# Performance work log

Hardware: AMD Instinct MI355X
Metric: run time of the kernel (lower is better)

## Reference

```python
import jax, jax.numpy as jnp
import numpy as np

B, D, T, BINS = 8, 768, 16384, 1024

def setup_inputs() -> dict:
    key = jax.random.key(0)
    k1, k2, k3, k4 = jax.random.split(key, 4)
    ssl_content = jax.random.normal(k1, (B, D, T), dtype=jnp.float32)
    conv_w = jax.random.normal(k2, (D, D, 2), dtype=jnp.float32) * 0.02  # Conv1d(768,768,k=2,s=2) weight [out,in,k]
    conv_b = jax.random.normal(k3, (D,), dtype=jnp.float32) * 0.02
    codebook = jax.random.normal(k4, (BINS, D), dtype=jnp.float32)
    return {"ssl_content": ssl_content, "conv_w": conv_w, "conv_b": conv_b, "codebook": codebook}

def reference(ssl_content, conv_w, conv_b, codebook):
    # ssl_proj: Conv1d(D, D, kernel_size=2, stride=2), no padding
    ssl = jax.lax.conv_general_dilated(
        ssl_content, conv_w, window_strides=(2,), padding='VALID',
        dimension_numbers=('NCH', 'OIH', 'NCH')) + conv_b[None, :, None]  # [B, D, T//2]
    x = jnp.transpose(ssl, (0, 2, 1))            # b d n -> b n d : [B, T', D]
    b, tq, d = x.shape
    flat = x.reshape(-1, d)                      # [B*T', D]
    # Euclidean codebook search: argmin_k ||flat - codebook[k]||^2
    d2 = (jnp.sum(flat * flat, axis=-1, keepdims=True)
          - 2.0 * (flat @ codebook.T)
          + jnp.sum(codebook * codebook, axis=-1))  # [B*T', BINS]
    codes = jnp.argmin(d2, axis=-1).reshape(b, tq)  # n_q=1 -> indices for quantizer 0: [B, T']
    prompt = codes[0][None, :]                   # codes[0,0].unsqueeze(0) -> [1, T']
    return prompt
```

## Files before the change

kernel.cpp:

```cpp
#include <hip/hip_runtime.h>

#define D    768
#define T    16384
#define TQ   8192
#define BINS 1024
#define K1   1536
#define NKA  (K1 / 32)
#define NKS  (D / 32)
#define FRAG 1024

typedef _Float16 f16;
typedef _Float16 h8 __attribute__((ext_vector_type(8)));
typedef float    f32x4 __attribute__((ext_vector_type(4)));


__device__ __forceinline__ void gl_lds16(const void* g, void* l) {
    __builtin_amdgcn_global_load_lds(
        (const __attribute__((address_space(1))) void*)g,
        (__attribute__((address_space(3))) void*)l, 16, 0, 0);
}

__global__ __launch_bounds__(64) void cnorm_kernel(const float* __restrict__ cb,
                                                   float* __restrict__ cnorm) {
    int bin  = blockIdx.x;
    int lane = threadIdx.x;
    const float* row = cb + bin * D;
    float s = 0.f;
    for (int k = lane; k < D; k += 64) { float v = row[k]; s += v * v; }
    #pragma unroll
    for (int off = 32; off > 0; off >>= 1) s += __shfl_down(s, off);
    if (lane == 0) cnorm[bin] = s;
}

__global__ __launch_bounds__(256) void pack_b_kernel(
    const float* __restrict__ src, f16* __restrict__ hi, f16* __restrict__ lo,
    int K, int nfrag) {
    int wid = threadIdx.x >> 6, lane = threadIdx.x & 63;
    int fid = blockIdx.x * 4 + wid;
    if (fid >= nfrag) return;
    int nk = K >> 5;
    int r16 = fid / nk, kblk = fid - r16 * nk;
    int row = r16 * 16 + (lane & 15);
    int k0  = kblk * 32 + 8 * (lane >> 4);
    const float* s = src + (size_t)row * K + k0;
    float4 v0 = *(const float4*)s;
    float4 v1 = *(const float4*)(s + 4);
    float vv[8] = {v0.x, v0.y, v0.z, v0.w, v1.x, v1.y, v1.z, v1.w};
    h8 vh, vl;
    #pragma unroll
    for (int j = 0; j < 8; ++j) {
        f16 h = (f16)vv[j];
        vh[j] = h;
        vl[j] = (f16)((vv[j] - (float)h) * 2048.f);
    }
    size_t off = ((size_t)fid * 64 + lane) * 8;
    *(h8*)&hi[off] = vh;
    *(h8*)&lo[off] = vl;
}

__global__ __launch_bounds__(256) void pack_a_kernel(const float* __restrict__ ssl,
                                                     f16* __restrict__ hi,
                                                     f16* __restrict__ lo) {
    int wid = threadIdx.x >> 6, lane = threadIdx.x & 63;
    int kblk = blockIdx.x;
    int l15 = lane & 15, lk = lane >> 4;
    #pragma unroll
    for (int q = 0; q < 2; ++q) {
        int tblk = blockIdx.y * 8 + wid * 2 + q;
        int tp = tblk * 16 + l15;
        int i0 = kblk * 16 + 4 * lk;
        float vv[8];
        #pragma unroll
        for (int ii = 0; ii < 4; ++ii) {
            float2 v = *(const float2*)&ssl[(size_t)(i0 + ii) * T + 2 * tp];
            vv[2 * ii]     = v.x;
            vv[2 * ii + 1] = v.y;
        }
        h8 vh, vl;
        #pragma unroll
        for (int j = 0; j < 8; ++j) {
            f16 h = (f16)vv[j];
            vh[j] = h;
            vl[j] = (f16)((vv[j] - (float)h) * 2048.f);
        }
        size_t off = ((size_t)(tblk * NKA + kblk) * 64 + lane) * 8;
        *(h8*)&hi[off] = vh;
        *(h8*)&lo[off] = vl;
    }
}

__global__ __launch_bounds__(256, 2) void conv_mfma_kernel(
    const f16* __restrict__ Ah, const f16* __restrict__ Al,
    const f16* __restrict__ Bh, const f16* __restrict__ Bl,
    const float* __restrict__ bias,
    f16* __restrict__ Xhi, f16* __restrict__ Xlo)
{
    __shared__ __align__(16) char smem[32768];
    int tid = threadIdx.x, lane = tid & 63, wid = tid >> 6;
    int wm = wid >> 1, wn = wid & 1;
    int l15 = lane & 15, lk = lane >> 4;
    int mb = blockIdx.y * 128, nb = blockIdx.x * 128;
    int mb16 = mb >> 4, nb16 = nb >> 4;

    const f16* gsrc; int blk16;
    if      (wid == 0) { gsrc = Ah; blk16 = mb16; }
    else if (wid == 1) { gsrc = Al; blk16 = mb16; }
    else if (wid == 2) { gsrc = Bh; blk16 = nb16; }
    else               { gsrc = Bl; blk16 = nb16; }
    const char* gw = (const char*)gsrc + (size_t)blk16 * NKA * FRAG + lane * 16;
    char* lw = smem + wid * 8192;

    const f32x4 zero4 = {0.f, 0.f, 0.f, 0.f};
    f32x4 acc[4][4];
    #pragma unroll
    for (int i = 0; i < 4; ++i)
        #pragma unroll
        for (int j = 0; j < 4; ++j) acc[i][j] = zero4;

    for (int kblk = 0; kblk < NKA; ++kblk) {
        __syncthreads();
        #pragma unroll
        for (int f = 0; f < 8; ++f)
            gl_lds16(gw + (size_t)(f * NKA + kblk) * FRAG, lw + f * FRAG);
        __syncthreads();
        h8 ah[4], al[4];
        #pragma unroll
        for (int mf = 0; mf < 4; ++mf) {
            int fo = (wm * 4 + mf) * FRAG + lane * 16;
            ah[mf] = *(const h8*)(smem + fo);
            al[mf] = *(const h8*)(smem + 8192 + fo);
        }
        #pragma unroll
        for (int nf = 0; nf < 4; ++nf) {
            int fo = (wn * 4 + nf) * FRAG + lane * 16;
            h8 bh = *(const h8*)(smem + 16384 + fo);
            h8 bl = *(const h8*)(smem + 24576 + fo);
            #pragma unroll
            for (int mf = 0; mf < 4; ++mf) {
                acc[mf][nf] = __builtin_amdgcn_mfma_f32_16x16x32_f16(ah[mf], bh, acc[mf][nf], 0, 0, 0);
                f32x4 t = __builtin_amdgcn_mfma_f32_16x16x32_f16(ah[mf], bl, zero4, 0, 0, 0);
                t = __builtin_amdgcn_mfma_f32_16x16x32_f16(al[mf], bh, t, 0, 0, 0);
                acc[mf][nf] += t * 4.8828125e-4f;
            }
        }
    }

    float* sb = (float*)smem;
    float bv[4];
    #pragma unroll
    for (int nf = 0; nf < 4; ++nf) bv[nf] = bias[nb + wn * 64 + nf * 16 + l15];
    #pragma unroll
    for (int s = 0; s < 4; ++s) {
        __syncthreads();
        if (wm == (s >> 1)) {
            #pragma unroll
            for (int mh = 0; mh < 2; ++mh) {
                int mf = (s & 1) * 2 + mh;
                int srow = mh * 16 + lk * 4;
                #pragma unroll
                for (int nf = 0; nf < 4; ++nf) {
                    int scol = wn * 64 + nf * 16 + l15;
                    #pragma unroll
                    for (int r = 0; r < 4; ++r)
                        sb[(srow + r) * 132 + scol] = acc[mf][nf][r] + bv[nf];
                }
            }
        }
        __syncthreads();
        #pragma unroll
        for (int h = 0; h < 2; ++h) {
            int f = wid * 2 + h;
            int tl = f & 1, dbl = f >> 1;
            int srow = tl * 16 + l15;
            int sd   = dbl * 32 + 8 * lk;
            float vv[8];
            #pragma unroll
            for (int j = 0; j < 8; ++j) vv[j] = sb[srow * 132 + sd + j];
            h8 vh, vl;
            #pragma unroll
            for (int j = 0; j < 8; ++j) {
                f16 hh = (f16)vv[j];
                vh[j] = hh;
                vl[j] = (f16)((vv[j] - (float)hh) * 2048.f);
            }
            int tblk_g = mb16 + s * 2 + tl;
            int dblk_g = (nb >> 5) + dbl;
            size_t off = ((size_t)(tblk_g * NKS + dblk_g) * 64 + lane) * 8;
            *(h8*)&Xhi[off] = vh;
            *(h8*)&Xlo[off] = vl;
        }
    }
}

__global__ __launch_bounds__(256, 2) void score_mfma_kernel(
    const f16* __restrict__ Ah, const f16* __restrict__ Al,
    const f16* __restrict__ Bh, const f16* __restrict__ Bl,
    const float* __restrict__ cnorm,
    float* __restrict__ pval, int* __restrict__ pidx)
{
    __shared__ __align__(16) char smem[32768];
    int tid = threadIdx.x, lane = tid & 63, wid = tid >> 6;
    int wm = wid >> 1, wn = wid & 1;
    int l15 = lane & 15, lk = lane >> 4;
    int mb = blockIdx.y * 128, nb = blockIdx.x * 128;
    int mb16 = mb >> 4, nb16 = nb >> 4;

    const f16* gsrc; int blk16;
    if      (wid == 0) { gsrc = Ah; blk16 = mb16; }
    else if (wid == 1) { gsrc = Al; blk16 = mb16; }
    else if (wid == 2) { gsrc = Bh; blk16 = nb16; }
    else               { gsrc = Bl; blk16 = nb16; }
    const char* gw = (const char*)gsrc + (size_t)blk16 * NKS * FRAG + lane * 16;
    char* lw = smem + wid * 8192;

    const f32x4 zero4 = {0.f, 0.f, 0.f, 0.f};
    f32x4 acc[4][4];
    #pragma unroll
    for (int i = 0; i < 4; ++i)
        #pragma unroll
        for (int j = 0; j < 4; ++j) acc[i][j] = zero4;

    for (int kblk = 0; kblk < NKS; ++kblk) {
        __syncthreads();
        #pragma unroll
        for (int f = 0; f < 8; ++f)
            gl_lds16(gw + (size_t)(f * NKS + kblk) * FRAG, lw + f * FRAG);
        __syncthreads();
        h8 ah[4], al[4];
        #pragma unroll
        for (int mf = 0; mf < 4; ++mf) {
            int fo = (wm * 4 + mf) * FRAG + lane * 16;
            ah[mf] = *(const h8*)(smem + fo);
            al[mf] = *(const h8*)(smem + 8192 + fo);
        }
        #pragma unroll
        for (int nf = 0; nf < 4; ++nf) {
            int fo = (wn * 4 + nf) * FRAG + lane * 16;
            h8 bh = *(const h8*)(smem + 16384 + fo);
            h8 bl = *(const h8*)(smem + 24576 + fo);
            #pragma unroll
            for (int mf = 0; mf < 4; ++mf) {
                acc[mf][nf] = __builtin_amdgcn_mfma_f32_16x16x32_f16(ah[mf], bh, acc[mf][nf], 0, 0, 0);
                f32x4 t = __builtin_amdgcn_mfma_f32_16x16x32_f16(ah[mf], bl, zero4, 0, 0, 0);
                t = __builtin_amdgcn_mfma_f32_16x16x32_f16(al[mf], bh, t, 0, 0, 0);
                acc[mf][nf] += t * 4.8828125e-4f;
            }
        }
    }
    float cn[4];
    #pragma unroll
    for (int nf = 0; nf < 4; ++nf) cn[nf] = cnorm[nb + wn * 64 + nf * 16 + l15];
    int slice = blockIdx.x * 2 + wn;
    #pragma unroll
    for (int mf = 0; mf < 4; ++mf) {
        #pragma unroll
        for (int r = 0; r < 4; ++r) {
            float v = 3.4e38f; int ix = 0;
            #pragma unroll
            for (int nf = 0; nf < 4; ++nf) {
                float sc = cn[nf] - 2.f * acc[mf][nf][r];
                int col = nb + wn * 64 + nf * 16 + l15;
                if (sc < v) { v = sc; ix = col; }
            }
            #pragma unroll
            for (int off = 8; off > 0; off >>= 1) {
                float ov = __shfl_xor(v, off);
                int   oi = __shfl_xor(ix, off);
                if (ov < v || (ov == v && oi < ix)) { v = ov; ix = oi; }
            }
            if (l15 == 0) {
                int row = mb + wm * 64 + mf * 16 + lk * 4 + r;
                pval[row * 16 + slice] = v;
                pidx[row * 16 + slice] = ix;
            }
        }
    }
}

__global__ __launch_bounds__(256) void argmin_final_kernel(
    const float* __restrict__ pval, const int* __restrict__ pidx,
    int* __restrict__ out)
{
    int r = blockIdx.x * 256 + threadIdx.x;
    float best = 3.4e38f; int bi = 0;
    #pragma unroll
    for (int s = 0; s < 16; ++s) {
        float v = pval[r * 16 + s];
        if (v < best) { best = v; bi = pidx[r * 16 + s]; }
    }
    out[r] = bi;
}

extern "C" void kernel_launch(void* const* d_in, const int* in_sizes, int n_in,
                              void* d_out, int out_size, void* d_ws, size_t ws_size,
                              hipStream_t stream) {
    const float* ssl = (const float*)d_in[0];
    const float* W   = (const float*)d_in[1];
    const float* bia = (const float*)d_in[2];
    const float* cb  = (const float*)d_in[3];
    int* out = (int*)d_out;

    char* p = (char*)d_ws;
    float* cnorm = (float*)p;  p += 4096;
    f16* Whi  = (f16*)p;  p += (size_t)D * K1 * 2;
    f16* Wlo  = (f16*)p;  p += (size_t)D * K1 * 2;
    f16* CBhi = (f16*)p;  p += (size_t)BINS * D * 2;
    f16* CBlo = (f16*)p;  p += (size_t)BINS * D * 2;
    f16* Ahi  = (f16*)p;  p += (size_t)TQ * K1 * 2;
    f16* Alo  = (f16*)p;  p += (size_t)TQ * K1 * 2;
    f16* Xhi  = (f16*)p;  p += (size_t)TQ * D * 2;
    f16* Xlo  = (f16*)p;  p += (size_t)TQ * D * 2;
    float* pval = (float*)p;  p += (size_t)TQ * 16 * 4;
    int*   pidx = (int*)p;    p += (size_t)TQ * 16 * 4;

    cnorm_kernel<<<BINS, 64, 0, stream>>>(cb, cnorm);
    pack_b_kernel<<<(48 * 48) / 4, 256, 0, stream>>>(W, Whi, Wlo, K1, 48 * 48);
    pack_b_kernel<<<(64 * 24) / 4, 256, 0, stream>>>(cb, CBhi, CBlo, D, 64 * 24);
    pack_a_kernel<<<dim3(NKA, TQ / 128), 256, 0, stream>>>(ssl, Ahi, Alo);
    conv_mfma_kernel<<<dim3(D / 128, TQ / 128), 256, 0, stream>>>(
        Ahi, Alo, Whi, Wlo, bia, Xhi, Xlo);
    score_mfma_kernel<<<dim3(BINS / 128, TQ / 128), 256, 0, stream>>>(
        Xhi, Xlo, CBhi, CBlo, cnorm, pval, pidx);
    argmin_final_kernel<<<TQ / 256, 256, 0, stream>>>(pval, pidx, out);
}
```

Baseline: 587.7 us.

## Double-buffer LDS tiles and accumulate correction terms in separate MFMA accumulators

Both GEMM kernels (conv and score) now use two LDS buffers, so the global-to-LDS load for the next k-block is issued before computing on the current one. This replaces two barriers per iteration with one. The hi/lo correction products are also accumulated in a second accumulator array and scaled once in the epilogue, instead of zero-init MFMAs plus a vector multiply-add every step. This doubles accumulator registers and LDS per block (64KB), which may reduce occupancy below the launch-bounds target of 2 blocks per CU.

Result: faster. 562.0 us (-4.4%).

```diff
diff --git a/kernel.cpp b/kernel.cpp
--- a/kernel.cpp
+++ b/kernel.cpp
@@ -95,7 +95,7 @@
     const float* __restrict__ bias,
     f16* __restrict__ Xhi, f16* __restrict__ Xlo)
 {
-    __shared__ __align__(16) char smem[32768];
+    __shared__ __align__(16) char smem[65536];
     int tid = threadIdx.x, lane = tid & 63, wid = tid >> 6;
     int wm = wid >> 1, wn = wid & 1;
     int l15 = lane & 15, lk = lane >> 4;
@@ -108,41 +108,51 @@
     else if (wid == 2) { gsrc = Bh; blk16 = nb16; }
     else               { gsrc = Bl; blk16 = nb16; }
     const char* gw = (const char*)gsrc + (size_t)blk16 * NKA * FRAG + lane * 16;
-    char* lw = smem + wid * 8192;
+    char* lw0 = smem + wid * 8192;
+    char* lw1 = smem + 32768 + wid * 8192;
 
     const f32x4 zero4 = {0.f, 0.f, 0.f, 0.f};
-    f32x4 acc[4][4];
+    f32x4 acc[4][4], acc2[4][4];
     #pragma unroll
     for (int i = 0; i < 4; ++i)
         #pragma unroll
-        for (int j = 0; j < 4; ++j) acc[i][j] = zero4;
-
+        for (int j = 0; j < 4; ++j) { acc[i][j] = zero4; acc2[i][j] = zero4; }
+
+    #pragma unroll
+    for (int f = 0; f < 8; ++f)
+        gl_lds16(gw + (size_t)(f * NKA) * FRAG, lw0 + f * FRAG);
+    __syncthreads();
+
+    int cur = 0;
     for (int kblk = 0; kblk < NKA; ++kblk) {
-        __syncthreads();
-        #pragma unroll
-        for (int f = 0; f < 8; ++f)
-            gl_lds16(gw + (size_t)(f * NKA + kblk) * FRAG, lw + f * FRAG);
-        __syncthreads();
+        if (kblk + 1 < NKA) {
+            char* lwn = cur ? lw0 : lw1;
+            #pragma unroll
+            for (int f = 0; f < 8; ++f)
+                gl_lds16(gw + (size_t)(f * NKA + kblk + 1) * FRAG, lwn + f * FRAG);
+        }
+        const char* base = smem + cur * 32768;
         h8 ah[4], al[4];
         #pragma unroll
         for (int mf = 0; mf < 4; ++mf) {
             int fo = (wm * 4 + mf) * FRAG + lane * 16;
-            ah[mf] = *(const h8*)(smem + fo);
-            al[mf] = *(const h8*)(smem + 8192 + fo);
+            ah[mf] = *(const h8*)(base + fo);
+            al[mf] = *(const h8*)(base + 8192 + fo);
         }
         #pragma unroll
         for (int nf = 0; nf < 4; ++nf) {
             int fo = (wn * 4 + nf) * FRAG + lane * 16;
-            h8 bh = *(const h8*)(smem + 16384 + fo);
-            h8 bl = *(const h8*)(smem + 24576 + fo);
+            h8 bh = *(const h8*)(base + 16384 + fo);
+            h8 bl = *(const h8*)(base + 24576 + fo);
             #pragma unroll
             for (int mf = 0; mf < 4; ++mf) {
-                acc[mf][nf] = __builtin_amdgcn_mfma_f32_16x16x32_f16(ah[mf], bh, acc[mf][nf], 0, 0, 0);
-                f32x4 t = __builtin_amdgcn_mfma_f32_16x16x32_f16(ah[mf], bl, zero4, 0, 0, 0);
-                t = __builtin_amdgcn_mfma_f32_16x16x32_f16(al[mf], bh, t, 0, 0, 0);
-                acc[mf][nf] += t * 4.8828125e-4f;
-            }
-        }
+                acc [mf][nf] = __builtin_amdgcn_mfma_f32_16x16x32_f16(ah[mf], bh, acc [mf][nf], 0, 0, 0);
+                acc2[mf][nf] = __builtin_amdgcn_mfma_f32_16x16x32_f16(ah[mf], bl, acc2[mf][nf], 0, 0, 0);
+                acc2[mf][nf] = __builtin_amdgcn_mfma_f32_16x16x32_f16(al[mf], bh, acc2[mf][nf], 0, 0, 0);
+            }
+        }
+        __syncthreads();
+        cur ^= 1;
     }
 
     float* sb = (float*)smem;
@@ -162,7 +172,8 @@
                     int scol = wn * 64 + nf * 16 + l15;
                     #pragma unroll
                     for (int r = 0; r < 4; ++r)
-                        sb[(srow + r) * 132 + scol] = acc[mf][nf][r] + bv[nf];
+                        sb[(srow + r) * 132 + scol] =
+                            acc[mf][nf][r] + acc2[mf][nf][r] * 4.8828125e-4f + bv[nf];
                 }
             }
         }
@@ -198,7 +209,7 @@
     const float* __restrict__ cnorm,
     float* __restrict__ pval, int* __restrict__ pidx)
 {
-    __shared__ __align__(16) char smem[32768];
+    __shared__ __align__(16) char smem[65536];
     int tid = threadIdx.x, lane = tid & 63, wid = tid >> 6;
     int wm = wid >> 1, wn = wid & 1;
     int l15 = lane & 15, lk = lane >> 4;
@@ -211,41 +222,51 @@
     else if (wid == 2) { gsrc = Bh; blk16 = nb16; }
     else               { gsrc = Bl; blk16 = nb16; }
     const char* gw = (const char*)gsrc + (size_t)blk16 * NKS * FRAG + lane * 16;
-    char* lw = smem + wid * 8192;
+    char* lw0 = smem + wid * 8192;
+    char* lw1 = smem + 32768 + wid * 8192;
 
     const f32x4 zero4 = {0.f, 0.f, 0.f, 0.f};
-    f32x4 acc[4][4];
+    f32x4 acc[4][4], acc2[4][4];
     #pragma unroll
     for (int i = 0; i < 4; ++i)
         #pragma unroll
-        for (int j = 0; j < 4; ++j) acc[i][j] = zero4;
-
+        for (int j = 0; j < 4; ++j) { acc[i][j] = zero4; acc2[i][j] = zero4; }
+
+    #pragma unroll
+    for (int f = 0; f < 8; ++f)
+        gl_lds16(gw + (size_t)(f * NKS) * FRAG, lw0 + f * FRAG);
+    __syncthreads();
+
+    int cur = 0;
     for (int kblk = 0; kblk < NKS; ++kblk) {
-        __syncthreads();
-        #pragma unroll
-        for (int f = 0; f < 8; ++f)
-            gl_lds16(gw + (size_t)(f * NKS + kblk) * FRAG, lw + f * FRAG);
-        __syncthreads();
+        if (kblk + 1 < NKS) {
+            char* lwn = cur ? lw0 : lw1;
+            #pragma unroll
+            for (int f = 0; f < 8; ++f)
+                gl_lds16(gw + (size_t)(f * NKS + kblk + 1) * FRAG, lwn + f * FRAG);
+        }
+        const char* base = smem + cur * 32768;
         h8 ah[4], al[4];
         #pragma unroll
         for (int mf = 0; mf < 4; ++mf) {
             int fo = (wm * 4 + mf) * FRAG + lane * 16;
-            ah[mf] = *(const h8*)(smem + fo);
-            al[mf] = *(const h8*)(smem + 8192 + fo);
+            ah[mf] = *(const h8*)(base + fo);
+            al[mf] = *(const h8*)(base + 8192 + fo);
         }
         #pragma unroll
         for (int nf = 0; nf < 4; ++nf) {
             int fo = (wn * 4 + nf) * FRAG + lane * 16;
-            h8 bh = *(const h8*)(smem + 16384 + fo);
-            h8 bl = *(const h8*)(smem + 24576 + fo);
+            h8 bh = *(const h8*)(base + 16384 + fo);
+            h8 bl = *(const h8*)(base + 24576 + fo);
             #pragma unroll
             for (int mf = 0; mf < 4; ++mf) {
-                acc[mf][nf] = __builtin_amdgcn_mfma_f32_16x16x32_f16(ah[mf], bh, acc[mf][nf], 0, 0, 0);
-                f32x4 t = __builtin_amdgcn_mfma_f32_16x16x32_f16(ah[mf], bl, zero4, 0, 0, 0);
-                t = __builtin_amdgcn_mfma_f32_16x16x32_f16(al[mf], bh, t, 0, 0, 0);
-                acc[mf][nf] += t * 4.8828125e-4f;
-            }
-        }
+                acc [mf][nf] = __builtin_amdgcn_mfma_f32_16x16x32_f16(ah[mf], bh, acc [mf][nf], 0, 0, 0);
+                acc2[mf][nf] = __builtin_amdgcn_mfma_f32_16x16x32_f16(ah[mf], bl, acc2[mf][nf], 0, 0, 0);
+                acc2[mf][nf] = __builtin_amdgcn_mfma_f32_16x16x32_f16(al[mf], bh, acc2[mf][nf], 0, 0, 0);
+            }
+        }
+        __syncthreads();
+        cur ^= 1;
     }
     float cn[4];
     #pragma unroll
@@ -258,7 +279,8 @@
             float v = 3.4e38f; int ix = 0;
             #pragma unroll
             for (int nf = 0; nf < 4; ++nf) {
-                float sc = cn[nf] - 2.f * acc[mf][nf][r];
+                float dot = acc[mf][nf][r] + acc2[mf][nf][r] * 4.8828125e-4f;
+                float sc = cn[nf] - 2.f * dot;
                 int col = nb + wn * 64 + nf * 16 + l15;
                 if (sc < v) { v = sc; ix = col; }
             }
```
